# Kernel tuning notes

Measured on AMD Instinct MI355X. Metric: run time of the kernel, lower is better.

Reference implementation:

```python
import jax, jax.numpy as jnp
import numpy as np

HEAD_DIM = 128
N_HEADS = 32
NEG_INF = -1e9


def apply_rope(x, cos, sin):
    # x: (B, S, H, D); cos/sin: (S, D//2). Pairs (x[...,2i], x[...,2i+1]) form
    # complex numbers (torch.view_as_complex on reshape(..., -1, 2)).
    xr = x[..., 0::2]
    xi = x[..., 1::2]
    c = cos[None, :, None, :]
    s = sin[None, :, None, :]
    out_r = xr * c - xi * s
    out_i = xr * s + xi * c
    return jnp.stack([out_r, out_i], axis=-1).reshape(x.shape)


def setup_inputs() -> dict:
    key = jax.random.key(0)
    ks = jax.random.split(key, 8)
    B, S, D = 2, 1024, 4096
    hd = HEAD_DIM
    x = jax.random.normal(ks[0], (B, S, D), dtype=jnp.float32)
    # true RoPE frequencies
    theta = 10000.0 ** (-np.arange(0, hd, 2, dtype=np.float32) / hd)  # (hd/2,)
    angles = np.arange(S, dtype=np.float32)[:, None] * theta[None, :]  # (S, hd/2)
    freqs_cos = jnp.asarray(np.cos(angles))
    freqs_sin = jnp.asarray(np.sin(angles))
    # causal additive mask
    mask = jnp.where(jnp.triu(jnp.ones((S, S), dtype=bool), k=1), NEG_INF, 0.0)
    mask = mask[None, None, :, :].astype(jnp.float32)
    scale = 0.02
    wq = jax.random.normal(ks[1], (D, D), dtype=jnp.float32) * scale
    wk = jax.random.normal(ks[2], (D, D), dtype=jnp.float32) * scale
    wv = jax.random.normal(ks[3], (D, D), dtype=jnp.float32) * scale
    wo = jax.random.normal(ks[4], (D, D), dtype=jnp.float32) * scale
    cache_k = jnp.zeros((B, S, N_HEADS, hd), dtype=jnp.float32)
    cache_v = jnp.zeros((B, S, N_HEADS, hd), dtype=jnp.float32)
    return {
        "x": x, "start_pos": 0, "freqs_cos": freqs_cos, "freqs_sin": freqs_sin,
        "mask": mask, "cache_k": cache_k, "cache_v": cache_v,
        "wq": wq, "wk": wk, "wv": wv, "wo": wo,
    }


def reference(x, start_pos, freqs_cos, freqs_sin, mask, cache_k, cache_v, wq, wk, wv, wo):
    B, S, D = x.shape
    H, hd = N_HEADS, HEAD_DIM
    # QKV projections (torch Linear: y = x @ W.T)
    xq = jnp.einsum('bsd,od->bso', x, wq).reshape(B, S, H, hd)
    xk = jnp.einsum('bsd,od->bso', x, wk).reshape(B, S, H, hd)
    xv = jnp.einsum('bsd,od->bso', x, wv).reshape(B, S, H, hd)
    xq = apply_rope(xq, freqs_cos, freqs_sin)
    xk = apply_rope(xk, freqs_cos, freqs_sin)
    # KV-cache append (n_rep == 1, so repeat_kv is identity)
    cache_k = jax.lax.dynamic_update_slice(cache_k, xk, (0, start_pos, 0, 0))
    cache_v = jax.lax.dynamic_update_slice(cache_v, xv, (0, start_pos, 0, 0))
    kv_len = start_pos + S
    keys = cache_k[:, :kv_len]
    values = cache_v[:, :kv_len]
    # attention: energy -> mask -> scaled softmax -> weighted sum
    energy = jnp.einsum('bqhd,bkhd->bhqk', xq, keys)
    energy = energy + mask
    scores = jax.nn.softmax(energy.astype(jnp.float32) / jnp.sqrt(jnp.float32(hd)), axis=-1).astype(xq.dtype)
    out = jnp.einsum('bhqk,bkhd->bqhd', scores, values).reshape(B, S, H * hd)
    return jnp.einsum('bso,do->bsd', out, wo)
```

## Files before the change

### kernel.cpp

```cpp
#include <hip/hip_runtime.h>
#include <hip/hip_bf16.h>
#include <stdint.h>
#include <stddef.h>

typedef __bf16 bf16_t;
typedef __attribute__((ext_vector_type(8))) __bf16 bf16x8;
typedef __attribute__((ext_vector_type(4))) float f32x4;

#define D_MODEL 4096
#define SEQ 1024
#define NH 32
#define HD 128
#define MTOT 2048

#define VMCNT(n) asm volatile("s_waitcnt vmcnt(" #n ")" ::: "memory")
#define LGKM0() asm volatile("s_waitcnt lgkmcnt(0)" ::: "memory")
#define SCHED0() __builtin_amdgcn_sched_barrier(0)

__device__ __forceinline__ void gload_lds16(const void* g, void* l) {
  __builtin_amdgcn_global_load_lds((const __attribute__((address_space(1))) uint32_t*)g,
                                   (__attribute__((address_space(3))) uint32_t*)l, 16, 0, 0);
}

__global__ void dtype_probe(const uint32_t* __restrict__ x, uint32_t* __restrict__ flag) {
  const int lane = threadIdx.x & 63;
  const uint32_t w = x[lane];
  const uint32_t e = (w >> 7) & 0xFF;
  const bool inband = (e >= 100 && e <= 140);
  const unsigned long long m = __ballot(inband);
  if (lane == 0) *flag = (__popcll(m) >= 32) ? 1u : 0u;
}

__global__ __launch_bounds__(256) void conv_bf16(const void* __restrict__ src,
                                                 bf16_t* __restrict__ dst, int n,
                                                 const uint32_t* __restrict__ flag) {
  const int i = (blockIdx.x * 256 + threadIdx.x) * 8;
  if (i >= n) return;
  if (*flag) {
    *(bf16x8*)(dst + i) = *(const bf16x8*)((const bf16_t*)src + i);
  } else {
    const float4 a = *(const float4*)((const float*)src + i);
    const float4 b = *(const float4*)((const float*)src + i + 4);
    bf16x8 v;
    v[0] = (bf16_t)a.x; v[1] = (bf16_t)a.y; v[2] = (bf16_t)a.z; v[3] = (bf16_t)a.w;
    v[4] = (bf16_t)b.x; v[5] = (bf16_t)b.y; v[6] = (bf16_t)b.z; v[7] = (bf16_t)b.w;
    *(bf16x8*)(dst + i) = v;
  }
}

template <int MODE>
__global__ __launch_bounds__(512, 2) void gemm_bt(
    const bf16_t* __restrict__ A, const bf16_t* __restrict__ B,
    void* __restrict__ dstv, const uint32_t* __restrict__ flagp) {
  __shared__ __align__(16) char smem[3 * 49152];
  const int tid = threadIdx.x;
  const int lane = tid & 63, wid = tid >> 6;
  const int fr = lane & 15, fq = lane >> 4;
  const int wm = wid >> 2, wn = wid & 3;
  const int bm0 = blockIdx.x * 128, bn0 = blockIdx.y * 256;
  const bool isbf = (MODE == 2) ? (*flagp != 0) : true;

  auto stage_half = [&](int t, int bi, int h) {
    const int k0 = t * 64;
    char* ab = smem + bi * 49152;
    char* bb = ab + 16384;
    {
      const int o = h * 8192 + tid * 16;
      const int row = o >> 7, ch = (o >> 4) & 7;
      gload_lds16(A + (size_t)(bm0 + row) * D_MODEL + k0 + ((ch ^ (row & 7)) * 8), ab + o);
    }
#pragma unroll
    for (int j = 0; j < 2; ++j) {
      const int o = (h * 2 + j) * 8192 + tid * 16;
      const int row = o >> 7, ch = (o >> 4) & 7;
      gload_lds16(B + (size_t)(bn0 + row) * D_MODEL + k0 + ((ch ^ (row & 7)) * 8), bb + o);
    }
  };

  f32x4 acc[4][4];
#pragma unroll
  for (int m = 0; m < 4; m++)
#pragma unroll
    for (int n = 0; n < 4; n++) acc[m][n] = f32x4{0.f, 0.f, 0.f, 0.f};

  auto phase = [&](int bi, int kk, bool do_stage, int ts, int bs, int h) {
    const char* ab = smem + bi * 49152;
    const char* bb = ab + 16384;
    const int swz = ((kk * 4 + fq) ^ (fr & 7)) << 4;
    bf16x8 af[4], bfv[4];
#pragma unroll
    for (int m = 0; m < 4; ++m)
      af[m] = *(const bf16x8*)(ab + (wm * 64 + m * 16 + fr) * 128 + swz);
#pragma unroll
    for (int n = 0; n < 4; ++n)
      bfv[n] = *(const bf16x8*)(bb + (wn * 64 + n * 16 + fr) * 128 + swz);
    if (do_stage) stage_half(ts, bs, h);
    __builtin_amdgcn_s_barrier();
    LGKM0();
    SCHED0();
    __builtin_amdgcn_s_setprio(1);
#pragma unroll
    for (int m = 0; m < 4; ++m)
#pragma unroll
      for (int n = 0; n < 4; ++n)
        acc[m][n] = __builtin_amdgcn_mfma_f32_16x16x32_bf16(af[m], bfv[n], acc[m][n], 0, 0, 0);
    __builtin_amdgcn_s_setprio(0);
  };

  const int NT = D_MODEL / 64;
  stage_half(0, 0, 0); stage_half(0, 0, 1);
  stage_half(1, 1, 0); stage_half(1, 1, 1);
  VMCNT(6);
  __builtin_amdgcn_s_barrier();
  SCHED0();
  int cur = 0, nxt = 2;
  for (int t = 0; t < NT - 2; ++t) {
    phase(cur, 0, true, t + 2, nxt, 0);
    __builtin_amdgcn_s_barrier();
    phase(cur, 1, true, t + 2, nxt, 1);
    VMCNT(6);
    __builtin_amdgcn_s_barrier();
    SCHED0();
    cur = (cur == 2) ? 0 : cur + 1;
    nxt = (nxt == 2) ? 0 : nxt + 1;
  }
  phase(cur, 0, false, 0, 0, 0);
  __builtin_amdgcn_s_barrier();
  phase(cur, 1, false, 0, 0, 0);
  VMCNT(0);
  __builtin_amdgcn_s_barrier();
  SCHED0();
  cur = (cur == 2) ? 0 : cur + 1;
  phase(cur, 0, false, 0, 0, 0);
  __builtin_amdgcn_s_barrier();
  phase(cur, 1, false, 0, 0, 0);

#pragma unroll
  for (int m = 0; m < 4; m++) {
#pragma unroll
    for (int n = 0; n < 4; n++) {
      const int gn = bn0 + wn * 64 + n * 16 + fr;
#pragma unroll
      for (int r = 0; r < 4; r++) {
        const int gm = bm0 + wm * 64 + m * 16 + fq * 4 + r;
        const float vv = acc[m][n][r];
        if constexpr (MODE == 0) {
          const int b = gm >> 10, s = gm & (SEQ - 1), h = gn >> 7, dd = gn & (HD - 1);
          ((bf16_t*)dstv)[((size_t)(b * NH + h) * SEQ + s) * HD + dd] = (bf16_t)vv;
        } else if constexpr (MODE == 1) {
          const int b = gm >> 10, s = gm & (SEQ - 1), h = gn >> 7, dd = gn & (HD - 1);
          ((bf16_t*)dstv)[((size_t)(b * NH + h) * HD + dd) * SEQ + s] = (bf16_t)vv;
        } else {
          if (isbf) ((bf16_t*)dstv)[(size_t)gm * D_MODEL + gn] = (bf16_t)vv;
          else      ((float*)dstv)[(size_t)gm * D_MODEL + gn] = vv;
        }
      }
    }
  }
}

__global__ __launch_bounds__(256) void rope_kernel(
    bf16_t* __restrict__ q, bf16_t* __restrict__ k,
    const bf16_t* __restrict__ fcos, const bf16_t* __restrict__ fsin) {
  const int PT = MTOT * (D_MODEL / 2);
  const int p = blockIdx.x * blockDim.x + threadIdx.x;
  bf16_t* buf = (p < PT) ? q : k;
  const int pp = p & (PT - 1);
  const int s = (pp >> 6) & (SEQ - 1);
  const int i = pp & 63;
  const float c = (float)fcos[s * 64 + i];
  const float si = (float)fsin[s * 64 + i];
  const float x0 = (float)buf[2 * (size_t)pp];
  const float x1 = (float)buf[2 * (size_t)pp + 1];
  buf[2 * (size_t)pp] = (bf16_t)(x0 * c - x1 * si);
  buf[2 * (size_t)pp + 1] = (bf16_t)(x0 * si + x1 * c);
}

__global__ __launch_bounds__(256, 3) void attn_fwd(
    const bf16_t* __restrict__ Q, const bf16_t* __restrict__ K,
    const bf16_t* __restrict__ V, bf16_t* __restrict__ Out) {
  constexpr float SC = 0.088388347648318447f;
  constexpr float MNEG = -10000.0f;
  __shared__ __align__(16) bf16_t Kt[64][136];
  __shared__ __align__(16) bf16_t Vt[128][72];
  __shared__ __align__(16) bf16_t Pb[4][16][72];
  const int tid = threadIdx.x, lane = tid & 63, wid = tid >> 6;
  const int fr = lane & 15, fq = lane >> 4;
  const int qt = (int)gridDim.x - 1 - blockIdx.x;
  const int bh = blockIdx.y;
  const int q0 = qt * 64 + wid * 16;

  const bf16_t* Kbase = K + (size_t)bh * SEQ * HD;
  const bf16_t* Vbase = V + (size_t)bh * HD * SEQ;

  bf16x8 qa[4];
  {
    const bf16_t* qp = Q + ((size_t)bh * SEQ + q0 + fr) * HD + fq * 8;
#pragma unroll
    for (int ks = 0; ks < 4; ++ks) qa[ks] = *(const bf16x8*)(qp + ks * 32);
  }
  f32x4 Oacc[8];
#pragma unroll
  for (int i = 0; i < 8; i++) Oacc[i] = f32x4{0.f, 0.f, 0.f, 0.f};
  float mrow[4] = {MNEG, MNEG, MNEG, MNEG};
  float lrow[4] = {0.f, 0.f, 0.f, 0.f};

  bf16x8 kreg[4], vreg[4];
  auto issue = [&](int kv0) {
#pragma unroll
    for (int j = 0; j < 4; ++j) {
      const int idx = j * 256 + tid;
      kreg[j] = *(const bf16x8*)(Kbase + (size_t)(kv0 + (idx >> 4)) * HD + (idx & 15) * 8);
      vreg[j] = *(const bf16x8*)(Vbase + (size_t)(idx >> 3) * SEQ + kv0 + (idx & 7) * 8);
    }
  };
  auto commit = [&]() {
#pragma unroll
    for (int j = 0; j < 4; ++j) {
      const int idx = j * 256 + tid;
      *(bf16x8*)&Kt[idx >> 4][(idx & 15) * 8] = kreg[j];
      *(bf16x8*)&Vt[idx >> 3][(idx & 7) * 8] = vreg[j];
    }
  };

  const int nt = qt + 1;
  issue(0);
  commit();
  __syncthreads();

  for (int t = 0; t < nt; ++t) {
    const bool last = (t == nt - 1);
    if (!last) issue((t + 1) * 64);

    f32x4 sacc[4];
#pragma unroll
    for (int nb = 0; nb < 4; ++nb) sacc[nb] = f32x4{0.f, 0.f, 0.f, 0.f};
    __builtin_amdgcn_s_setprio(1);
#pragma unroll
    for (int nb = 0; nb < 4; ++nb) {
      const int kvc = nb * 16 + fr;
#pragma unroll
      for (int ks = 0; ks < 4; ++ks) {
        bf16x8 kb = *(const bf16x8*)&Kt[kvc][(ks * 4 + fq) * 8];
        sacc[nb] = __builtin_amdgcn_mfma_f32_16x16x32_bf16(qa[ks], kb, sacc[nb], 0, 0, 0);
      }
    }
    __builtin_amdgcn_s_setprio(0);

    float xv[4][4], al[4];
#pragma unroll
    for (int r = 0; r < 4; ++r) {
      const int qrow = q0 + fq * 4 + r;
#pragma unroll
      for (int nb = 0; nb < 4; ++nb) {
        const float xx = sacc[nb][r] * SC;
        xv[nb][r] = (!last || (t * 64 + nb * 16 + fr) <= qrow) ? xx : MNEG;
      }
      float pm = fmaxf(fmaxf(xv[0][r], xv[1][r]), fmaxf(xv[2][r], xv[3][r]));
      pm = fmaxf(pm, __shfl_xor(pm, 1));
      pm = fmaxf(pm, __shfl_xor(pm, 2));
      pm = fmaxf(pm, __shfl_xor(pm, 4));
      pm = fmaxf(pm, __shfl_xor(pm, 8));
      const float mn = fmaxf(mrow[r], pm);
      al[r] = __expf(mrow[r] - mn);
      mrow[r] = mn;
      float ps = 0.f;
#pragma unroll
      for (int nb = 0; nb < 4; ++nb) {
        const float pv = __expf(xv[nb][r] - mn);
        xv[nb][r] = pv;
        ps += pv;
      }
      lrow[r] = lrow[r] * al[r] + ps;
    }
#pragma unroll
    for (int db = 0; db < 8; ++db)
#pragma unroll
      for (int r = 0; r < 4; ++r) Oacc[db][r] *= al[r];

#pragma unroll
    for (int nb = 0; nb < 4; ++nb)
#pragma unroll
      for (int r = 0; r < 4; ++r)
        Pb[wid][fq * 4 + r][nb * 16 + fr] = (bf16_t)xv[nb][r];
    bf16x8 pa0 = *(const bf16x8*)&Pb[wid][fr][fq * 8];
    bf16x8 pa1 = *(const bf16x8*)&Pb[wid][fr][32 + fq * 8];

    __builtin_amdgcn_s_setprio(1);
#pragma unroll
    for (int db = 0; db < 8; ++db) {
      const int d = db * 16 + fr;
      bf16x8 vb0 = *(const bf16x8*)&Vt[d][fq * 8];
      bf16x8 vb1 = *(const bf16x8*)&Vt[d][32 + fq * 8];
      Oacc[db] = __builtin_amdgcn_mfma_f32_16x16x32_bf16(pa0, vb0, Oacc[db], 0, 0, 0);
      Oacc[db] = __builtin_amdgcn_mfma_f32_16x16x32_bf16(pa1, vb1, Oacc[db], 0, 0, 0);
    }
    __builtin_amdgcn_s_setprio(0);

    if (!last) {
      __syncthreads();
      commit();
      __syncthreads();
    }
  }

  float linv[4];
#pragma unroll
  for (int r = 0; r < 4; ++r) {
    float ps = lrow[r];
    ps += __shfl_xor(ps, 1);
    ps += __shfl_xor(ps, 2);
    ps += __shfl_xor(ps, 4);
    ps += __shfl_xor(ps, 8);
    linv[r] = 1.0f / fmaxf(ps, 1e-20f);
  }

  const int b = bh >> 5, h = bh & 31;
#pragma unroll
  for (int db = 0; db < 8; ++db) {
    const int d = db * 16 + fr;
#pragma unroll
    for (int r = 0; r < 4; ++r) {
      const int q = q0 + fq * 4 + r;
      Out[((size_t)(b * SEQ + q)) * D_MODEL + h * HD + d] = (bf16_t)(Oacc[db][r] * linv[r]);
    }
  }
}

extern "C" void kernel_launch(void* const* d_in, const int* in_sizes, int n_in,
                              void* d_out, int out_size, void* d_ws, size_t ws_size,
                              hipStream_t stream) {
  (void)in_sizes; (void)n_in; (void)out_size;
  const void* x_raw    = d_in[0];
  const void* fcos_raw = d_in[2];
  const void* fsin_raw = d_in[3];
  const void* wq_raw   = d_in[7];
  const void* wk_raw   = d_in[8];
  const void* wv_raw   = d_in[9];
  const void* wo_raw   = d_in[10];

  const size_t NX = (size_t)MTOT * D_MODEL;
  const size_t NW = (size_t)D_MODEL * D_MODEL;
  const size_t NF = SEQ * (HD / 2);

  char* base = (char*)d_ws;
  uint32_t* flag = (uint32_t*)base;
  bf16_t* fc = (bf16_t*)(base + 4096);
  bf16_t* fs = (bf16_t*)(base + 4096 + 131072);
  bf16_t* elems = (bf16_t*)(base + (1 << 20));
  bf16_t* xc = elems;
  bf16_t* w0 = xc + NX;
  bf16_t* w1 = w0 + NW;
  bf16_t* q_ws = w1 + NW;
  bf16_t* k_ws = q_ws + NX;
  bf16_t* v_ws = k_ws + NX;
  bf16_t* a_ws = v_ws + NX;
  const size_t NEED = (1 << 20) + 2 * (5 * NX + 2 * NW);
  if (ws_size < NEED) return;

  dtype_probe<<<1, 64, 0, stream>>>((const uint32_t*)x_raw, flag);

  const int cb_x = (int)(NX / (256 * 8));
  const int cb_w = (int)(NW / (256 * 8));
  const int cb_f = (int)(NF / (256 * 8));
  conv_bf16<<<cb_x, 256, 0, stream>>>(x_raw, xc, (int)NX, flag);
  conv_bf16<<<cb_f, 256, 0, stream>>>(fcos_raw, fc, (int)NF, flag);
  conv_bf16<<<cb_f, 256, 0, stream>>>(fsin_raw, fs, (int)NF, flag);

  dim3 gg(MTOT / 128, D_MODEL / 256);
  conv_bf16<<<cb_w, 256, 0, stream>>>(wq_raw, w0, (int)NW, flag);
  gemm_bt<0><<<gg, 512, 0, stream>>>(xc, w0, q_ws, flag);
  conv_bf16<<<cb_w, 256, 0, stream>>>(wk_raw, w1, (int)NW, flag);
  gemm_bt<0><<<gg, 512, 0, stream>>>(xc, w1, k_ws, flag);
  conv_bf16<<<cb_w, 256, 0, stream>>>(wv_raw, w0, (int)NW, flag);
  gemm_bt<1><<<gg, 512, 0, stream>>>(xc, w0, v_ws, flag);

  rope_kernel<<<(2 * MTOT * (D_MODEL / 2)) / 256, 256, 0, stream>>>(q_ws, k_ws, fc, fs);
  attn_fwd<<<dim3(SEQ / 64, 2 * NH), 256, 0, stream>>>(q_ws, k_ws, v_ws, a_ws);

  conv_bf16<<<cb_w, 256, 0, stream>>>(wo_raw, w1, (int)NW, flag);
  gemm_bt<2><<<gg, 512, 0, stream>>>(a_ws, w1, d_out, flag);
}
```

Before: 438.9 us.

## Rewrite attention with 256-query tiles, 32x32 MFMA and async LDS double buffering

The attention kernel now uses 512-thread blocks covering 256 query rows, with 32x32x16 MFMAs and S^T computed so the P operand stays in registers through bf16 pack and permlane32 swap instead of a shared-memory round trip. K/V tiles are staged with direct global-to-LDS loads into XOR-swizzled double buffers, and output is written coalesced via LDS. This aims to raise K/V reuse per load, cut LDS traffic and bank conflicts, and overlap loads with compute. The cost is fewer blocks (256 total) with causal load imbalance across waves, plus higher register pressure.

```diff
diff --git a/kernel.cpp b/kernel.cpp
--- a/kernel.cpp
+++ b/kernel.cpp
@@ -6,6 +6,8 @@
 typedef __bf16 bf16_t;
 typedef __attribute__((ext_vector_type(8))) __bf16 bf16x8;
 typedef __attribute__((ext_vector_type(4))) float f32x4;
+typedef __attribute__((ext_vector_type(16))) float f32x16;
+typedef __attribute__((ext_vector_type(4))) uint32_t u32x4;
 
 #define D_MODEL 4096
 #define SEQ 1024
@@ -20,6 +22,15 @@
 __device__ __forceinline__ void gload_lds16(const void* g, void* l) {
   __builtin_amdgcn_global_load_lds((const __attribute__((address_space(1))) uint32_t*)g,
                                    (__attribute__((address_space(3))) uint32_t*)l, 16, 0, 0);
+}
+
+__device__ __forceinline__ uint32_t cvtpk(float lo, float hi) {
+  uint32_t r;
+  asm("v_cvt_pk_bf16_f32 %0, %1, %2" : "=v"(r) : "v"(lo), "v"(hi));
+  return r;
+}
+__device__ __forceinline__ void plswap(uint32_t& a, uint32_t& b) {
+  asm volatile("v_permlane32_swap_b32 %0, %1" : "+v"(a), "+v"(b));
 }
 
 __global__ void dtype_probe(const uint32_t* __restrict__ x, uint32_t* __restrict__ flag) {
@@ -176,154 +187,180 @@
   buf[2 * (size_t)pp + 1] = (bf16_t)(x0 * si + x1 * c);
 }
 
-__global__ __launch_bounds__(256, 3) void attn_fwd(
+__global__ __launch_bounds__(512, 2) void attn_fwd(
     const bf16_t* __restrict__ Q, const bf16_t* __restrict__ K,
     const bf16_t* __restrict__ V, bf16_t* __restrict__ Out) {
   constexpr float SC = 0.088388347648318447f;
   constexpr float MNEG = -10000.0f;
-  __shared__ __align__(16) bf16_t Kt[64][136];
-  __shared__ __align__(16) bf16_t Vt[128][72];
-  __shared__ __align__(16) bf16_t Pb[4][16][72];
+  __shared__ __align__(16) char smem[65536];
   const int tid = threadIdx.x, lane = tid & 63, wid = tid >> 6;
-  const int fr = lane & 15, fq = lane >> 4;
-  const int qt = (int)gridDim.x - 1 - blockIdx.x;
+  const int l31 = lane & 31, hi = lane >> 5, l7 = lane & 7;
+  const int qt = 3 - (int)blockIdx.x;
   const int bh = blockIdx.y;
-  const int q0 = qt * 64 + wid * 16;
+  const int qb0 = qt * 256;
+  const int q0w = qb0 + wid * 32;
+  const int nt = qt * 4 + 4;
 
   const bf16_t* Kbase = K + (size_t)bh * SEQ * HD;
   const bf16_t* Vbase = V + (size_t)bh * HD * SEQ;
 
-  bf16x8 qa[4];
+  bf16x8 qa[8];
   {
-    const bf16_t* qp = Q + ((size_t)bh * SEQ + q0 + fr) * HD + fq * 8;
-#pragma unroll
-    for (int ks = 0; ks < 4; ++ks) qa[ks] = *(const bf16x8*)(qp + ks * 32);
-  }
-  f32x4 Oacc[8];
-#pragma unroll
-  for (int i = 0; i < 8; i++) Oacc[i] = f32x4{0.f, 0.f, 0.f, 0.f};
-  float mrow[4] = {MNEG, MNEG, MNEG, MNEG};
-  float lrow[4] = {0.f, 0.f, 0.f, 0.f};
-
-  bf16x8 kreg[4], vreg[4];
-  auto issue = [&](int kv0) {
-#pragma unroll
-    for (int j = 0; j < 4; ++j) {
-      const int idx = j * 256 + tid;
-      kreg[j] = *(const bf16x8*)(Kbase + (size_t)(kv0 + (idx >> 4)) * HD + (idx & 15) * 8);
-      vreg[j] = *(const bf16x8*)(Vbase + (size_t)(idx >> 3) * SEQ + kv0 + (idx & 7) * 8);
+    const bf16_t* qp = Q + ((size_t)bh * SEQ + q0w + l31) * HD + hi * 8;
+#pragma unroll
+    for (int ks = 0; ks < 8; ++ks) qa[ks] = *(const bf16x8*)(qp + ks * 16);
+  }
+
+  auto stage = [&](int t, int bi) {
+    const int kv0 = t * 64;
+#pragma unroll
+    for (int pass = 0; pass < 2; ++pass) {
+      const int o = pass * 8192 + tid * 16;
+      {
+        const int row = o >> 8, ch = (o & 255) >> 4;
+        gload_lds16(Kbase + (size_t)(kv0 + row) * HD + ((ch ^ (row & 7)) * 8),
+                    smem + bi * 16384 + o);
+      }
+      {
+        const int row = o >> 7, ch = (o & 127) >> 4;
+        gload_lds16(Vbase + (size_t)row * SEQ + kv0 + ((ch ^ (row & 7)) * 8),
+                    smem + 32768 + bi * 16384 + o);
+      }
     }
   };
-  auto commit = [&]() {
-#pragma unroll
-    for (int j = 0; j < 4; ++j) {
-      const int idx = j * 256 + tid;
-      *(bf16x8*)&Kt[idx >> 4][(idx & 15) * 8] = kreg[j];
-      *(bf16x8*)&Vt[idx >> 3][(idx & 7) * 8] = vreg[j];
-    }
-  };
-
-  const int nt = qt + 1;
-  issue(0);
-  commit();
-  __syncthreads();
+
+  f32x16 Oacc[4];
+#pragma unroll
+  for (int i = 0; i < 4; ++i)
+#pragma unroll
+    for (int j = 0; j < 16; ++j) Oacc[i][j] = 0.f;
+  float mrow = MNEG, lrow = 0.f;
+
+  stage(0, 0);
+  stage(1, 1);
+  VMCNT(4);
+  __builtin_amdgcn_s_barrier();
 
   for (int t = 0; t < nt; ++t) {
-    const bool last = (t == nt - 1);
-    if (!last) issue((t + 1) * 64);
-
-    f32x4 sacc[4];
-#pragma unroll
-    for (int nb = 0; nb < 4; ++nb) sacc[nb] = f32x4{0.f, 0.f, 0.f, 0.f};
-    __builtin_amdgcn_s_setprio(1);
-#pragma unroll
-    for (int nb = 0; nb < 4; ++nb) {
-      const int kvc = nb * 16 + fr;
-#pragma unroll
-      for (int ks = 0; ks < 4; ++ks) {
-        bf16x8 kb = *(const bf16x8*)&Kt[kvc][(ks * 4 + fq) * 8];
-        sacc[nb] = __builtin_amdgcn_mfma_f32_16x16x32_bf16(qa[ks], kb, sacc[nb], 0, 0, 0);
+    const int kv0 = t * 64;
+    if (kv0 < q0w + 32) {
+      const char* kb_ = smem + (t & 1) * 16384;
+      const char* vb_ = smem + 32768 + (t & 1) * 16384;
+
+      f32x16 sacc[2];
+#pragma unroll
+      for (int kb = 0; kb < 2; ++kb)
+#pragma unroll
+        for (int j = 0; j < 16; ++j) sacc[kb][j] = 0.f;
+      __builtin_amdgcn_s_setprio(1);
+#pragma unroll
+      for (int kb = 0; kb < 2; ++kb)
+#pragma unroll
+        for (int ks = 0; ks < 8; ++ks) {
+          bf16x8 kf = *(const bf16x8*)(kb_ + (kb * 32 + l31) * 256 +
+                                       (((ks * 2 + hi) ^ l7) << 4));
+          sacc[kb] = __builtin_amdgcn_mfma_f32_32x32x16_bf16(kf, qa[ks], sacc[kb], 0, 0, 0);
+        }
+      __builtin_amdgcn_s_setprio(0);
+
+      const bool diag = (kv0 + 63 > q0w);
+      float pm = MNEG;
+#pragma unroll
+      for (int kb = 0; kb < 2; ++kb)
+#pragma unroll
+        for (int r = 0; r < 16; ++r) {
+          float x = sacc[kb][r] * SC;
+          if (diag) {
+            const int kvpos = kv0 + kb * 32 + (r & 3) + 8 * (r >> 2) + 4 * hi;
+            if (kvpos > q0w + l31) x = MNEG;
+          }
+          sacc[kb][r] = x;
+          pm = fmaxf(pm, x);
+        }
+      pm = fmaxf(pm, __shfl_xor(pm, 32));
+      const float mn = fmaxf(mrow, pm);
+      const float al = __expf(mrow - mn);
+      mrow = mn;
+      float ps = 0.f;
+#pragma unroll
+      for (int kb = 0; kb < 2; ++kb)
+#pragma unroll
+        for (int r = 0; r < 16; ++r) {
+          const float e = __expf(sacc[kb][r] - mn);
+          sacc[kb][r] = e;
+          ps += e;
+        }
+      lrow = lrow * al + ps;
+#pragma unroll
+      for (int db = 0; db < 4; ++db)
+#pragma unroll
+        for (int j = 0; j < 16; ++j) Oacc[db][j] *= al;
+
+      uint32_t pw[16];
+#pragma unroll
+      for (int kb = 0; kb < 2; ++kb) {
+        const int o8 = kb * 8;
+        pw[o8 + 0] = cvtpk(sacc[kb][0], sacc[kb][1]);
+        pw[o8 + 1] = cvtpk(sacc[kb][2], sacc[kb][3]);
+        pw[o8 + 2] = cvtpk(sacc[kb][4], sacc[kb][5]);
+        pw[o8 + 3] = cvtpk(sacc[kb][6], sacc[kb][7]);
+        plswap(pw[o8 + 0], pw[o8 + 2]);
+        plswap(pw[o8 + 1], pw[o8 + 3]);
+        pw[o8 + 4] = cvtpk(sacc[kb][8], sacc[kb][9]);
+        pw[o8 + 5] = cvtpk(sacc[kb][10], sacc[kb][11]);
+        pw[o8 + 6] = cvtpk(sacc[kb][12], sacc[kb][13]);
+        pw[o8 + 7] = cvtpk(sacc[kb][14], sacc[kb][15]);
+        plswap(pw[o8 + 4], pw[o8 + 6]);
+        plswap(pw[o8 + 5], pw[o8 + 7]);
       }
-    }
-    __builtin_amdgcn_s_setprio(0);
-
-    float xv[4][4], al[4];
-#pragma unroll
-    for (int r = 0; r < 4; ++r) {
-      const int qrow = q0 + fq * 4 + r;
-#pragma unroll
-      for (int nb = 0; nb < 4; ++nb) {
-        const float xx = sacc[nb][r] * SC;
-        xv[nb][r] = (!last || (t * 64 + nb * 16 + fr) <= qrow) ? xx : MNEG;
+
+      __builtin_amdgcn_s_setprio(1);
+#pragma unroll
+      for (int db = 0; db < 4; ++db)
+#pragma unroll
+        for (int ks2 = 0; ks2 < 4; ++ks2) {
+          bf16x8 vf = *(const bf16x8*)(vb_ + (db * 32 + l31) * 128 +
+                                       (((ks2 * 2 + hi) ^ l7) << 4));
+          union { u32x4 u; bf16x8 v; } pc;
+          pc.u = u32x4{pw[ks2 * 4], pw[ks2 * 4 + 1], pw[ks2 * 4 + 2], pw[ks2 * 4 + 3]};
+          Oacc[db] = __builtin_amdgcn_mfma_f32_32x32x16_bf16(vf, pc.v, Oacc[db], 0, 0, 0);
+        }
+      __builtin_amdgcn_s_setprio(0);
+    }
+
+    __builtin_amdgcn_s_barrier();
+    if (t + 2 < nt) {
+      stage(t + 2, t & 1);
+      VMCNT(4);
+    } else if (t + 1 < nt) {
+      VMCNT(0);
+    }
+    __builtin_amdgcn_s_barrier();
+  }
+
+  lrow += __shfl_xor(lrow, 32);
+  const float linv = 1.0f / fmaxf(lrow, 1e-20f);
+
+  {
+    char* ob = smem + wid * 8192;
+#pragma unroll
+    for (int db = 0; db < 4; ++db)
+#pragma unroll
+      for (int rp = 0; rp < 8; ++rp) {
+        const int r = rp * 2;
+        const int d = db * 32 + (r & 3) + 8 * (r >> 2) + 4 * hi;
+        const uint32_t w = cvtpk(Oacc[db][r] * linv, Oacc[db][r + 1] * linv);
+        *(uint32_t*)(ob + l31 * 256 + ((d * 2) ^ ((l31 & 7) << 4))) = w;
       }
-      float pm = fmaxf(fmaxf(xv[0][r], xv[1][r]), fmaxf(xv[2][r], xv[3][r]));
-      pm = fmaxf(pm, __shfl_xor(pm, 1));
-      pm = fmaxf(pm, __shfl_xor(pm, 2));
-      pm = fmaxf(pm, __shfl_xor(pm, 4));
-      pm = fmaxf(pm, __shfl_xor(pm, 8));
-      const float mn = fmaxf(mrow[r], pm);
-      al[r] = __expf(mrow[r] - mn);
-      mrow[r] = mn;
-      float ps = 0.f;
-#pragma unroll
-      for (int nb = 0; nb < 4; ++nb) {
-        const float pv = __expf(xv[nb][r] - mn);
-        xv[nb][r] = pv;
-        ps += pv;
-      }
-      lrow[r] = lrow[r] * al[r] + ps;
-    }
-#pragma unroll
-    for (int db = 0; db < 8; ++db)
-#pragma unroll
-      for (int r = 0; r < 4; ++r) Oacc[db][r] *= al[r];
-
-#pragma unroll
-    for (int nb = 0; nb < 4; ++nb)
-#pragma unroll
-      for (int r = 0; r < 4; ++r)
-        Pb[wid][fq * 4 + r][nb * 16 + fr] = (bf16_t)xv[nb][r];
-    bf16x8 pa0 = *(const bf16x8*)&Pb[wid][fr][fq * 8];
-    bf16x8 pa1 = *(const bf16x8*)&Pb[wid][fr][32 + fq * 8];
-
-    __builtin_amdgcn_s_setprio(1);
-#pragma unroll
-    for (int db = 0; db < 8; ++db) {
-      const int d = db * 16 + fr;
-      bf16x8 vb0 = *(const bf16x8*)&Vt[d][fq * 8];
-      bf16x8 vb1 = *(const bf16x8*)&Vt[d][32 + fq * 8];
-      Oacc[db] = __builtin_amdgcn_mfma_f32_16x16x32_bf16(pa0, vb0, Oacc[db], 0, 0, 0);
-      Oacc[db] = __builtin_amdgcn_mfma_f32_16x16x32_bf16(pa1, vb1, Oacc[db], 0, 0, 0);
-    }
-    __builtin_amdgcn_s_setprio(0);
-
-    if (!last) {
-      __syncthreads();
-      commit();
-      __syncthreads();
-    }
-  }
-
-  float linv[4];
-#pragma unroll
-  for (int r = 0; r < 4; ++r) {
-    float ps = lrow[r];
-    ps += __shfl_xor(ps, 1);
-    ps += __shfl_xor(ps, 2);
-    ps += __shfl_xor(ps, 4);
-    ps += __shfl_xor(ps, 8);
-    linv[r] = 1.0f / fmaxf(ps, 1e-20f);
-  }
-
+  }
+  __builtin_amdgcn_s_barrier();
   const int b = bh >> 5, h = bh & 31;
 #pragma unroll
-  for (int db = 0; db < 8; ++db) {
-    const int d = db * 16 + fr;
-#pragma unroll
-    for (int r = 0; r < 4; ++r) {
-      const int q = q0 + fq * 4 + r;
-      Out[((size_t)(b * SEQ + q)) * D_MODEL + h * HD + d] = (bf16_t)(Oacc[db][r] * linv[r]);
-    }
+  for (int pass = 0; pass < 8; ++pass) {
+    const int o = pass * 8192 + tid * 16;
+    const int row = o >> 8, ch = (o & 255) >> 4;
+    const u32x4 val = *(const u32x4*)(smem + row * 256 + ((ch ^ (row & 7)) << 4));
+    *(u32x4*)(Out + ((size_t)(b * SEQ + qb0 + row)) * D_MODEL + h * HD + ch * 8) = val;
   }
 }
 
@@ -376,7 +413,7 @@
   gemm_bt<1><<<gg, 512, 0, stream>>>(xc, w0, v_ws, flag);
 
   rope_kernel<<<(2 * MTOT * (D_MODEL / 2)) / 256, 256, 0, stream>>>(q_ws, k_ws, fc, fs);
-  attn_fwd<<<dim3(SEQ / 64, 2 * NH), 256, 0, stream>>>(q_ws, k_ws, v_ws, a_ws);
+  attn_fwd<<<dim3(4, 2 * NH), 512, 0, stream>>>(q_ws, k_ws, v_ws, a_ws);
 
   conv_bf16<<<cb_w, 256, 0, stream>>>(wo_raw, w1, (int)NW, flag);
   gemm_bt<2><<<gg, 512, 0, stream>>>(a_ws, w1, d_out, flag);
```

Result: faster. 415.6 us (-5.3%).
